# Kernel optimization log

Hardware: AMD Instinct MI355X
Metric: run time of the kernel (lower is better)

Reference implementation:

```python
import jax, jax.numpy as jnp
import numpy as np

B, T, D, U = 32, 2048, 512, 512

def setup_inputs() -> dict:
    key = jax.random.key(0)
    ks = jax.random.split(key, 7)
    s = 1.0 / np.sqrt(D)
    return {
        "query": jax.random.normal(ks[0], (B, D), jnp.float32),
        "values": jax.random.normal(ks[1], (B, T, D), jnp.float32),
        "W1": jax.random.normal(ks[2], (D, U), jnp.float32) * s,
        "b1": jnp.zeros((U,), jnp.float32),
        "W2": jax.random.normal(ks[3], (D, U), jnp.float32) * s,
        "b2": jnp.zeros((U,), jnp.float32),
        "V": jax.random.normal(ks[4], (U, 1), jnp.float32) * (1.0 / np.sqrt(U)),
        "bV": jnp.zeros((1,), jnp.float32),
    }

def reference(query, values, W1, b1, W2, b2, V, bV):
    # values: [B,T,D], query: [B,D]
    proj_v = jnp.einsum('btd,du->btu', values, W1) + b1          # [B,T,U]
    proj_q = (query @ W2 + b2)[:, None, :]                        # [B,1,U]
    score = jnp.tanh(proj_v + proj_q) @ V + bV                    # [B,T,1]
    attention_weights = jax.nn.softmax(score, axis=1)             # [B,T,1]
    context_vector = jnp.sum(attention_weights * values, axis=1)  # [B,D]
    return (context_vector, attention_weights)
```

## Files before the change

### kernel.cpp

```cpp
#include <hip/hip_runtime.h>
#include <hip/hip_bf16.h>
#include <math.h>

#define BB 32
#define TT 2048
#define DD 512
#define UU 512

typedef __attribute__((ext_vector_type(8))) short short8v;
typedef __attribute__((ext_vector_type(4))) float floatx4;
typedef __attribute__((ext_vector_type(8))) unsigned short ushort8v;
typedef __attribute__((ext_vector_type(4))) unsigned short ushort4v;

static __device__ inline unsigned short f2bf(float f) {
  __hip_bfloat16 h = __float2bfloat16(f);
  return *reinterpret_cast<unsigned short*>(&h);
}

static __device__ inline float fast_tanh(float x) {
  x = fminf(fmaxf(x, -15.f), 15.f);
  float e2 = __expf(2.f * x);
  return (e2 - 1.f) * __builtin_amdgcn_rcpf(e2 + 1.f);
}

__global__ __launch_bounds__(256) void pack_w1a_kernel(
    const float* __restrict__ W1, unsigned short* __restrict__ w1a) {
  __shared__ float Wf[32][132];
  const int kt = blockIdx.x, uc = blockIdx.y;
  const int tid = threadIdx.x;
  {
    const int k = tid >> 3;
    const int u16 = (tid & 7) * 16;
    const float* src = W1 + (size_t)(kt * 32 + k) * UU + uc * 128 + u16;
    #pragma unroll
    for (int q = 0; q < 4; ++q) {
      const float4 v = *(const float4*)(src + q * 4);
      Wf[k][u16 + q * 4 + 0] = v.x;
      Wf[k][u16 + q * 4 + 1] = v.y;
      Wf[k][u16 + q * 4 + 2] = v.z;
      Wf[k][u16 + q * 4 + 3] = v.w;
    }
  }
  __syncthreads();
  unsigned short* dst = w1a + (size_t)kt * 16384;
  #pragma unroll
  for (int s = 0; s < 2; ++s) {
    const int c = s * 256 + tid;
    const int kg = c >> 7;
    const int u = c & 127;
    ushort8v o;
    #pragma unroll
    for (int e = 0; e < 8; ++e) o[e] = f2bf(Wf[kg * 8 + e][u]);
    *(ushort8v*)(dst + ((size_t)kg * 512 + uc * 128 + u) * 8) = o;
  }
}

__global__ __launch_bounds__(256) void projq_kernel(
    const float* __restrict__ query, const float* __restrict__ W2,
    const float* __restrict__ b2, const float* __restrict__ b1,
    float* __restrict__ qb) {
  int b = blockIdx.x;
  int u = blockIdx.y * 256 + threadIdx.x;
  float acc = b2[u] + b1[u];
  const float* q = query + b * DD;
  #pragma unroll 16
  for (int d = 0; d < DD; ++d) acc += q[d] * W2[(size_t)d * UU + u];
  qb[b * UU + u] = acc;
}

#define SBM 64

__global__ __launch_bounds__(512, 4) void score_kernel(
    const float* __restrict__ values, const unsigned short* __restrict__ w1a,
    const float* __restrict__ qb, const float* __restrict__ V,
    float* __restrict__ score) {
  __shared__ __align__(16) unsigned short Bp[16][4][SBM][8];
  __shared__ float qv_lds[512];
  __shared__ float vv_lds[512];
  __shared__ float part[8][SBM];

  const int tid = threadIdx.x;
  const int row0 = blockIdx.x * SBM;
  const int b = row0 >> 11;
  const int lane = tid & 63;
  const int wid = tid >> 6;
  const int wu = wid * 64;
  const int fr = lane & 15;
  const int kg = lane >> 4;

  qv_lds[tid] = qb[b * UU + tid];
  vv_lds[tid] = V[tid];

  const int sm = tid >> 3;
  const int sj = tid & 7;
  const float* bsrc = values + (size_t)(row0 + sm) * DD + sj * 4;
  unsigned short* bdst = &Bp[0][sj >> 1][sm][(sj & 1) * 4];
  #pragma unroll
  for (int half = 0; half < 2; ++half) {
    float4 r[8];
    #pragma unroll
    for (int q = 0; q < 8; ++q)
      r[q] = *(const float4*)(bsrc + (size_t)(half * 8 + q) * 32);
    #pragma unroll
    for (int q = 0; q < 8; ++q) {
      ushort4v o = {f2bf(r[q].x), f2bf(r[q].y), f2bf(r[q].z), f2bf(r[q].w)};
      *(ushort4v*)(bdst + (size_t)(half * 8 + q) * 2048) = o;
    }
  }
  __syncthreads();

  const size_t aofs = (size_t)(kg * 512 + wu + fr) * 8;
  floatx4 acc[4][4] = {};
  short8v af[2][4];
  #pragma unroll
  for (int ju = 0; ju < 4; ++ju)
    af[0][ju] = *(const short8v*)(w1a + aofs + (size_t)ju * 128);

  #pragma unroll
  for (int t = 0; t < 16; ++t) {
    const int cur = t & 1;
    const int nxt = cur ^ 1;
    if (t + 1 < 16) {
      #pragma unroll
      for (int ju = 0; ju < 4; ++ju)
        af[nxt][ju] = *(const short8v*)(w1a + (size_t)(t + 1) * 16384 + aofs + (size_t)ju * 128);
    }
    #pragma unroll
    for (int jm = 0; jm < 4; ++jm) {
      const short8v bfv = *(const short8v*)&Bp[t][kg][jm * 16 + fr][0];
      #pragma unroll
      for (int ju = 0; ju < 4; ++ju)
        acc[ju][jm] = __builtin_amdgcn_mfma_f32_16x16x32_bf16(af[cur][ju], bfv, acc[ju][jm], 0, 0, 0);
    }
  }

  float pm[4] = {0.f, 0.f, 0.f, 0.f};
  #pragma unroll
  for (int ju = 0; ju < 4; ++ju) {
    const float4 qv = *(const float4*)&qv_lds[wu + ju * 16 + kg * 4];
    const float4 vv = *(const float4*)&vv_lds[wu + ju * 16 + kg * 4];
    const float qa[4] = {qv.x, qv.y, qv.z, qv.w};
    const float va[4] = {vv.x, vv.y, vv.z, vv.w};
    #pragma unroll
    for (int jm = 0; jm < 4; ++jm)
      #pragma unroll
      for (int reg = 0; reg < 4; ++reg)
        pm[jm] += fast_tanh(acc[ju][jm][reg] + qa[reg]) * va[reg];
  }
  #pragma unroll
  for (int jm = 0; jm < 4; ++jm) {
    pm[jm] += __shfl_xor(pm[jm], 16, 64);
    pm[jm] += __shfl_xor(pm[jm], 32, 64);
  }
  if (lane < 16) {
    #pragma unroll
    for (int jm = 0; jm < 4; ++jm) part[wid][jm * 16 + lane] = pm[jm];
  }
  __syncthreads();
  if (tid < SBM) {
    float s = 0.f;
    #pragma unroll
    for (int w = 0; w < 8; ++w) s += part[w][tid];
    score[row0 + tid] = s;
  }
}

__global__ __launch_bounds__(256) void softmax_kernel(
    const float* __restrict__ score, float* __restrict__ attn) {
  const int b = blockIdx.x;
  const int tid = threadIdx.x;
  __shared__ float red[256];

  float m = -INFINITY;
  for (int t = tid; t < TT; t += 256) m = fmaxf(m, score[b * TT + t]);
  red[tid] = m;
  __syncthreads();
  for (int s = 128; s > 0; s >>= 1) {
    if (tid < s) red[tid] = fmaxf(red[tid], red[tid + s]);
    __syncthreads();
  }
  const float bm = red[0];
  __syncthreads();

  float sum = 0.f;
  for (int t = tid; t < TT; t += 256) sum += __expf(score[b * TT + t] - bm);
  red[tid] = sum;
  __syncthreads();
  for (int s = 128; s > 0; s >>= 1) {
    if (tid < s) red[tid] += red[tid + s];
    __syncthreads();
  }
  const float inv = 1.f / red[0];
  __syncthreads();

  for (int t = tid; t < TT; t += 256)
    attn[b * TT + t] = __expf(score[b * TT + t] - bm) * inv;
}

#define CSPLIT 64
__global__ __launch_bounds__(128) void context1_kernel(
    const float* __restrict__ values, const float* __restrict__ attn,
    float* __restrict__ partial) {
  const int s = blockIdx.x;
  const int b = blockIdx.y;
  const int t0 = s * (TT / CSPLIT);
  const int d = threadIdx.x * 4;
  float4 a = {0.f, 0.f, 0.f, 0.f};
  #pragma unroll 4
  for (int t = t0; t < t0 + TT / CSPLIT; ++t) {
    const float w = attn[b * TT + t];
    const float4 v = *(const float4*)(values + (size_t)(b * TT + t) * DD + d);
    a.x += w * v.x; a.y += w * v.y; a.z += w * v.z; a.w += w * v.w;
  }
  *(float4*)(partial + ((size_t)s * BB + b) * DD + d) = a;
}

__global__ __launch_bounds__(128) void context2_kernel(
    const float* __restrict__ partial, float* __restrict__ ctx) {
  const int b = blockIdx.x;
  const int d = threadIdx.x * 4;
  float4 a = {0.f, 0.f, 0.f, 0.f};
  #pragma unroll 8
  for (int s = 0; s < CSPLIT; ++s) {
    const float4 p = *(const float4*)(partial + ((size_t)s * BB + b) * DD + d);
    a.x += p.x; a.y += p.y; a.z += p.z; a.w += p.w;
  }
  *(float4*)(ctx + (size_t)b * DD + d) = a;
}

extern "C" void kernel_launch(void* const* d_in, const int* in_sizes, int n_in,
                              void* d_out, int out_size, void* d_ws, size_t ws_size,
                              hipStream_t stream) {
  const float* query  = (const float*)d_in[0];
  const float* values = (const float*)d_in[1];
  const float* W1     = (const float*)d_in[2];
  const float* b1     = (const float*)d_in[3];
  const float* W2     = (const float*)d_in[4];
  const float* b2     = (const float*)d_in[5];
  const float* V      = (const float*)d_in[6];

  float* ctx  = (float*)d_out;
  float* attn = (float*)d_out + BB * DD;

  float* qb           = (float*)d_ws;
  float* score        = qb + BB * UU;
  unsigned short* w1a = (unsigned short*)(score + BB * TT);
  float* partial      = (float*)(w1a + (size_t)UU * DD);

  pack_w1a_kernel<<<dim3(16, 4), 256, 0, stream>>>(W1, w1a);
  projq_kernel<<<dim3(BB, UU / 256), 256, 0, stream>>>(query, W2, b2, b1, qb);

  score_kernel<<<(BB * TT) / SBM, 512, 0, stream>>>(values, w1a, qb, V, score);

  softmax_kernel<<<BB, 256, 0, stream>>>(score, attn);

  context1_kernel<<<dim3(CSPLIT, BB), 128, 0, stream>>>(values, attn, partial);
  context2_kernel<<<BB, 128, 0, stream>>>(partial, ctx);
}
```

Baseline: 99.63 us.

## Overlap second half of values tile load with first half of MFMA loop

Splits the staging of the values tile into LDS into two halves. Only the first half is converted and synced before compute starts; the second half's global loads are issued early and written to LDS at iteration 8, behind a mid-loop barrier. The W1 fragment prefetch also deepens from double to triple buffering, so loads run two steps ahead. This aims to hide global load latency behind MFMA work, at the cost of extra registers (r1 plus a third af buffer) that could lower occupancy or cause spills.

```diff
diff --git a/kernel.cpp b/kernel.cpp
--- a/kernel.cpp
+++ b/kernel.cpp
@@ -74,7 +74,7 @@
     const float* __restrict__ values, const unsigned short* __restrict__ w1a,
     const float* __restrict__ qb, const float* __restrict__ V,
     float* __restrict__ score) {
-  __shared__ __align__(16) unsigned short Bp[16][4][SBM][8];
+  __shared__ __align__(16) unsigned short Bp[2][8][4][SBM][8];
   __shared__ float qv_lds[512];
   __shared__ float vv_lds[512];
   __shared__ float part[8][SBM];
@@ -94,43 +94,61 @@
   const int sm = tid >> 3;
   const int sj = tid & 7;
   const float* bsrc = values + (size_t)(row0 + sm) * DD + sj * 4;
-  unsigned short* bdst = &Bp[0][sj >> 1][sm][(sj & 1) * 4];
-  #pragma unroll
-  for (int half = 0; half < 2; ++half) {
-    float4 r[8];
+  const int bofs = (sj >> 1) * (SBM * 8) + sm * 8 + (sj & 1) * 4;
+
+  {
+    float4 r0[8];
     #pragma unroll
     for (int q = 0; q < 8; ++q)
-      r[q] = *(const float4*)(bsrc + (size_t)(half * 8 + q) * 32);
+      r0[q] = *(const float4*)(bsrc + (size_t)q * 32);
     #pragma unroll
     for (int q = 0; q < 8; ++q) {
-      ushort4v o = {f2bf(r[q].x), f2bf(r[q].y), f2bf(r[q].z), f2bf(r[q].w)};
-      *(ushort4v*)(bdst + (size_t)(half * 8 + q) * 2048) = o;
-    }
-  }
-  __syncthreads();
+      ushort4v o = {f2bf(r0[q].x), f2bf(r0[q].y), f2bf(r0[q].z), f2bf(r0[q].w)};
+      *(ushort4v*)(&Bp[0][q][0][0][0] + bofs) = o;
+    }
+  }
 
   const size_t aofs = (size_t)(kg * 512 + wu + fr) * 8;
+  short8v af[3][4];
+  #pragma unroll
+  for (int ju = 0; ju < 4; ++ju) {
+    af[0][ju] = *(const short8v*)(w1a + aofs + (size_t)ju * 128);
+    af[1][ju] = *(const short8v*)(w1a + 16384 + aofs + (size_t)ju * 128);
+  }
+
+  __syncthreads();
+
+  float4 r1[8];
+  #pragma unroll
+  for (int q = 0; q < 8; ++q)
+    r1[q] = *(const float4*)(bsrc + (size_t)(8 + q) * 32);
+
   floatx4 acc[4][4] = {};
-  short8v af[2][4];
-  #pragma unroll
-  for (int ju = 0; ju < 4; ++ju)
-    af[0][ju] = *(const short8v*)(w1a + aofs + (size_t)ju * 128);
 
   #pragma unroll
   for (int t = 0; t < 16; ++t) {
-    const int cur = t & 1;
-    const int nxt = cur ^ 1;
-    if (t + 1 < 16) {
+    if (t == 8) {
+      #pragma unroll
+      for (int q = 0; q < 8; ++q) {
+        ushort4v o = {f2bf(r1[q].x), f2bf(r1[q].y), f2bf(r1[q].z), f2bf(r1[q].w)};
+        *(ushort4v*)(&Bp[1][q][0][0][0] + bofs) = o;
+      }
+      __syncthreads();
+    }
+
+    if (t + 2 < 16) {
       #pragma unroll
       for (int ju = 0; ju < 4; ++ju)
-        af[nxt][ju] = *(const short8v*)(w1a + (size_t)(t + 1) * 16384 + aofs + (size_t)ju * 128);
-    }
+        af[(t + 2) % 3][ju] =
+            *(const short8v*)(w1a + (size_t)(t + 2) * 16384 + aofs + (size_t)ju * 128);
+    }
+
     #pragma unroll
     for (int jm = 0; jm < 4; ++jm) {
-      const short8v bfv = *(const short8v*)&Bp[t][kg][jm * 16 + fr][0];
+      const short8v bfv = *(const short8v*)&Bp[t >> 3][t & 7][kg][jm * 16 + fr][0];
       #pragma unroll
       for (int ju = 0; ju < 4; ++ju)
-        acc[ju][jm] = __builtin_amdgcn_mfma_f32_16x16x32_bf16(af[cur][ju], bfv, acc[ju][jm], 0, 0, 0);
+        acc[ju][jm] = __builtin_amdgcn_mfma_f32_16x16x32_bf16(af[t % 3][ju], bfv, acc[ju][jm], 0, 0, 0);
     }
   }
 
```

Result: slower. 103.6 us (+3.9%).

## Pipeline score GEMM with triple-buffered direct global-to-LDS loads

Applied to the files above, without the earlier changes.

Replaces the upfront bf16 conversion of the whole 64x512 values tile into LDS with a 3-stage pipeline. Each K-step's W1 slice and fp32 values slice are loaded asynchronously with global_load_lds, under explicit vmcnt waits and barriers. Values are stored in LDS as fp32 with an XOR swizzle and converted to bf16 just before the MFMA, and A fragments are now read from LDS instead of straight from global memory. The aim is to overlap global latency with MFMA work. The cost is more LDS (about 120KB), which means lowering the launch bound to 2 blocks per CU, plus repeated per-step conversion work.

```diff
diff --git a/kernel.cpp b/kernel.cpp
--- a/kernel.cpp
+++ b/kernel.cpp
@@ -10,7 +10,6 @@
 typedef __attribute__((ext_vector_type(8))) short short8v;
 typedef __attribute__((ext_vector_type(4))) float floatx4;
 typedef __attribute__((ext_vector_type(8))) unsigned short ushort8v;
-typedef __attribute__((ext_vector_type(4))) unsigned short ushort4v;
 
 static __device__ inline unsigned short f2bf(float f) {
   __hip_bfloat16 h = __float2bfloat16(f);
@@ -21,6 +20,12 @@
   x = fminf(fmaxf(x, -15.f), 15.f);
   float e2 = __expf(2.f * x);
   return (e2 - 1.f) * __builtin_amdgcn_rcpf(e2 + 1.f);
+}
+
+static __device__ inline void gload16(const void* g, void* l) {
+  __builtin_amdgcn_global_load_lds(
+      (const __attribute__((address_space(1))) unsigned int*)g,
+      (__attribute__((address_space(3))) unsigned int*)(l), 16, 0, 0);
 }
 
 __global__ __launch_bounds__(256) void pack_w1a_kernel(
@@ -70,11 +75,12 @@
 
 #define SBM 64
 
-__global__ __launch_bounds__(512, 4) void score_kernel(
+__global__ __launch_bounds__(512, 2) void score_kernel(
     const float* __restrict__ values, const unsigned short* __restrict__ w1a,
     const float* __restrict__ qb, const float* __restrict__ V,
     float* __restrict__ score) {
-  __shared__ __align__(16) unsigned short Bp[16][4][SBM][8];
+  __shared__ __align__(16) unsigned short Aa[3][16384];
+  __shared__ __align__(16) float Bf[3][2048];
   __shared__ float qv_lds[512];
   __shared__ float vv_lds[512];
   __shared__ float part[8][SBM];
@@ -91,48 +97,69 @@
   qv_lds[tid] = qb[b * UU + tid];
   vv_lds[tid] = V[tid];
 
-  const int sm = tid >> 3;
-  const int sj = tid & 7;
-  const float* bsrc = values + (size_t)(row0 + sm) * DD + sj * 4;
-  unsigned short* bdst = &Bp[0][sj >> 1][sm][(sj & 1) * 4];
-  #pragma unroll
-  for (int half = 0; half < 2; ++half) {
-    float4 r[8];
-    #pragma unroll
-    for (int q = 0; q < 8; ++q)
-      r[q] = *(const float4*)(bsrc + (size_t)(half * 8 + q) * 32);
-    #pragma unroll
-    for (int q = 0; q < 8; ++q) {
-      ushort4v o = {f2bf(r[q].x), f2bf(r[q].y), f2bf(r[q].z), f2bf(r[q].w)};
-      *(ushort4v*)(bdst + (size_t)(half * 8 + q) * 2048) = o;
-    }
-  }
-  __syncthreads();
-
-  const size_t aofs = (size_t)(kg * 512 + wu + fr) * 8;
+  const int brow = tid >> 3;
+  const int bkq = (tid & 7) ^ (brow & 7);
+  const float* bsrc0 = values + (size_t)(row0 + brow) * DD + bkq * 4;
+
+  const char* abase = (const char*)w1a;
+
+  #define STAGE(T, P)                                                        \
+    {                                                                        \
+      const char* ak = abase + (size_t)(T) * 32768;                          \
+      char* al = (char*)&Aa[P][0];                                           \
+      gload16(ak + (0 * 512 + tid) * 16, al + (0 * 512 + tid) * 16);         \
+      gload16(ak + (1 * 512 + tid) * 16, al + (1 * 512 + tid) * 16);         \
+      gload16(ak + (2 * 512 + tid) * 16, al + (2 * 512 + tid) * 16);         \
+      gload16(ak + (3 * 512 + tid) * 16, al + (3 * 512 + tid) * 16);         \
+      gload16(bsrc0 + (T) * 32, (char*)&Bf[P][0] + tid * 16);                \
+    }
+
+  STAGE(0, 0)
+  STAGE(1, 1)
+  __builtin_amdgcn_sched_barrier(0);
+  asm volatile("s_waitcnt vmcnt(5) lgkmcnt(0)" ::: "memory");
+  __builtin_amdgcn_sched_barrier(0);
+  __builtin_amdgcn_s_barrier();
+
   floatx4 acc[4][4] = {};
-  short8v af[2][4];
-  #pragma unroll
-  for (int ju = 0; ju < 4; ++ju)
-    af[0][ju] = *(const short8v*)(w1a + aofs + (size_t)ju * 128);
 
   #pragma unroll
   for (int t = 0; t < 16; ++t) {
-    const int cur = t & 1;
-    const int nxt = cur ^ 1;
-    if (t + 1 < 16) {
+    const int p = t % 3;
+
+    if (t + 2 < 16) STAGE(t + 2, (t + 2) % 3)
+
+    short8v af[4];
+    #pragma unroll
+    for (int ju = 0; ju < 4; ++ju)
+      af[ju] = *(const short8v*)&Aa[p][(size_t)(kg * 512 + wu + ju * 16 + fr) * 8];
+    #pragma unroll
+    for (int jm = 0; jm < 4; ++jm) {
+      const int row = jm * 16 + fr;
+      const int p0 = row * 8 + ((2 * kg + 0) ^ (row & 7));
+      const int p1 = row * 8 + ((2 * kg + 1) ^ (row & 7));
+      const floatx4 f0 = *(const floatx4*)&Bf[p][p0 * 4];
+      const floatx4 f1 = *(const floatx4*)&Bf[p][p1 * 4];
+      const short8v bfv = {
+          (short)f2bf(f0[0]), (short)f2bf(f0[1]), (short)f2bf(f0[2]), (short)f2bf(f0[3]),
+          (short)f2bf(f1[0]), (short)f2bf(f1[1]), (short)f2bf(f1[2]), (short)f2bf(f1[3])};
       #pragma unroll
       for (int ju = 0; ju < 4; ++ju)
-        af[nxt][ju] = *(const short8v*)(w1a + (size_t)(t + 1) * 16384 + aofs + (size_t)ju * 128);
-    }
-    #pragma unroll
-    for (int jm = 0; jm < 4; ++jm) {
-      const short8v bfv = *(const short8v*)&Bp[t][kg][jm * 16 + fr][0];
-      #pragma unroll
-      for (int ju = 0; ju < 4; ++ju)
-        acc[ju][jm] = __builtin_amdgcn_mfma_f32_16x16x32_bf16(af[cur][ju], bfv, acc[ju][jm], 0, 0, 0);
-    }
-  }
+        acc[ju][jm] = __builtin_amdgcn_mfma_f32_16x16x32_bf16(af[ju], bfv, acc[ju][jm], 0, 0, 0);
+    }
+
+    if (t < 15) {
+      __builtin_amdgcn_sched_barrier(0);
+      if (t + 2 < 16) {
+        asm volatile("s_waitcnt vmcnt(5)" ::: "memory");
+      } else {
+        asm volatile("s_waitcnt vmcnt(0)" ::: "memory");
+      }
+      __builtin_amdgcn_sched_barrier(0);
+      __builtin_amdgcn_s_barrier();
+    }
+  }
+  #undef STAGE
 
   float pm[4] = {0.f, 0.f, 0.f, 0.f};
   #pragma unroll
```

New measurement: 118.2 us. 1.19x slower.
